# Optimization experiments

Hardware: AMD Instinct MI355X
Metric: run time of the kernel (lower is better)

The kernel has to match this reference:

```python
import jax, jax.numpy as jnp
import numpy as np

B, X, Y, Z = 8, 128, 128, 128


def setup_inputs() -> dict:
    key = jax.random.key(0)
    k1, k2 = jax.random.split(key)
    mu = jax.random.normal(k1, (B, X, Y, Z), dtype=jnp.float32)
    active = jax.random.uniform(k2, (B, X, Y, Z), dtype=jnp.float32)
    dx = jnp.ones((1,), dtype=jnp.float32)
    return {"mu": mu, "active": active, "dx": dx}


def _lap_kernel(mu, active, dx):
    # mu, active: [X, Y, Z] single-sample grids; dx: scalar
    mu_eff = mu * active
    lap = (jnp.roll(mu_eff, 1, 0) + jnp.roll(mu_eff, -1, 0)
           + jnp.roll(mu_eff, 1, 1) + jnp.roll(mu_eff, -1, 1)
           + jnp.roll(mu_eff, 1, 2) + jnp.roll(mu_eff, -1, 2)
           - 6.0 * mu_eff) / dx ** 2
    return lap * active


def reference(mu, active, dx):
    # Faithful to Node.proces_collection: gather fields by pattern, then
    # vmap the runnable with in_axes=(0, 0, None) over the batch axis.
    out = jax.vmap(_lap_kernel, in_axes=(0, 0, None))(mu, active, dx[0])
    return out
```

## Files before the change

kernel.cpp:

```cpp
#include <hip/hip_runtime.h>

#define NB 8
#define NX 128
#define NY 128
#define NZ 128

#define TY 8
#define TX 8
#define XC (NX / TX)
#define YT (NY / TY)
#define PLANE_ROWS (TY + 2)

__global__ __launch_bounds__(256) void lap_lds(
    const float* __restrict__ mu,
    const float* __restrict__ act,
    const float* __restrict__ dxp,
    float* __restrict__ out)
{
    __shared__ float e[3][PLANE_ROWS][NZ];

    const int tid = threadIdx.x;
    const int bid = blockIdx.x;
    const int xc = bid & (XC - 1);
    const int yt = (bid >> 4) & (YT - 1);
    const int b  = bid >> 8;

    const int x0 = xc * TX;
    const int y0 = yt * TY;
    const int planeYZ = NY * NZ;
    const int baseB = b * NX * planeYZ;

    const float dxv = dxp[0];
    const float inv = 1.0f / (dxv * dxv);

    const int r  = tid >> 5;
    const int zq = tid & 31;
    const int z0 = zq * 4;

    float4 A;
    float4 Bt;

    auto load_plane = [&](int gx, int slot, float4* keepA) {
        const int px = baseB + gx * planeYZ;
        {
            const int gIdx = px + (y0 + r) * NZ + z0;
            float4 m = *reinterpret_cast<const float4*>(mu + gIdx);
            float4 a = *reinterpret_cast<const float4*>(act + gIdx);
            *keepA = a;
            float4 ev = make_float4(m.x * a.x, m.y * a.y, m.z * a.z, m.w * a.w);
            *reinterpret_cast<float4*>(&e[slot][r + 1][z0]) = ev;
        }
        if (tid < 64) {
            const int hr = tid >> 5;
            const int hzq = tid & 31;
            const int gy = hr ? ((y0 + TY) & (NY - 1)) : ((y0 - 1) & (NY - 1));
            const int lr = hr ? (TY + 1) : 0;
            const int gIdx = px + gy * NZ + hzq * 4;
            float4 m = *reinterpret_cast<const float4*>(mu + gIdx);
            float4 a = *reinterpret_cast<const float4*>(act + gIdx);
            float4 ev = make_float4(m.x * a.x, m.y * a.y, m.z * a.z, m.w * a.w);
            *reinterpret_cast<float4*>(&e[slot][lr][hzq * 4]) = ev;
        }
    };

    load_plane((x0 - 1) & (NX - 1), 0, &Bt);
    load_plane(x0, 1, &A);

    for (int i = 0; i < TX; ++i) {
        const int sm = i % 3;
        const int sc = (i + 1) % 3;
        const int sp = (i + 2) % 3;

        load_plane((x0 + i + 1) & (NX - 1), sp, &Bt);
        __syncthreads();

        const int gx = x0 + i;
        const int px = baseB + gx * planeYZ;
        {
            float4 ec  = *reinterpret_cast<const float4*>(&e[sc][r + 1][z0]);
            float4 exm = *reinterpret_cast<const float4*>(&e[sm][r + 1][z0]);
            float4 exP = *reinterpret_cast<const float4*>(&e[sp][r + 1][z0]);
            float4 eym = *reinterpret_cast<const float4*>(&e[sc][r][z0]);
            float4 eyp = *reinterpret_cast<const float4*>(&e[sc][r + 2][z0]);
            float ezm = e[sc][r + 1][(z0 - 1) & (NZ - 1)];
            float ezp = e[sc][r + 1][(z0 + 4) & (NZ - 1)];
            float4 o;
            o.x = (exm.x + exP.x + eym.x + eyp.x + ezm + ec.y - 6.0f * ec.x) * inv * A.x;
            o.y = (exm.y + exP.y + eym.y + eyp.y + ec.x + ec.z - 6.0f * ec.y) * inv * A.y;
            o.z = (exm.z + exP.z + eym.z + eyp.z + ec.y + ec.w - 6.0f * ec.z) * inv * A.z;
            o.w = (exm.w + exP.w + eym.w + eyp.w + ec.z + ezp - 6.0f * ec.w) * inv * A.w;
            const int gIdx = px + (y0 + r) * NZ + z0;
            *reinterpret_cast<float4*>(out + gIdx) = o;
        }

        A = Bt;
        __syncthreads();
    }
}

extern "C" void kernel_launch(void* const* d_in, const int* in_sizes, int n_in,
                              void* d_out, int out_size, void* d_ws, size_t ws_size,
                              hipStream_t stream) {
    const float* mu  = (const float*)d_in[0];
    const float* act = (const float*)d_in[1];
    const float* dx  = (const float*)d_in[2];
    float* out = (float*)d_out;

    const int grid = NB * YT * XC;
    lap_lds<<<grid, 256, 0, stream>>>(mu, act, dx, out);
}
```

Before: 40.57 us.

## March x-planes in registers with double-buffered LDS and larger tiles

Each thread now keeps its previous, current and next x-plane values in registers instead of a triple-buffered LDS array. LDS is cut to a double buffer used only for y-neighbours, and z-neighbours come from warp shuffles. Tiles grow to 16x16 with 512 threads, which lowers the relative halo reload overhead. In exchange there is one fewer barrier per plane, more register pressure, fewer blocks in the grid, and the next-plane load is exposed within each iteration.

```diff
diff --git a/kernel.cpp b/kernel.cpp
--- a/kernel.cpp
+++ b/kernel.cpp
@@ -5,25 +5,25 @@
 #define NY 128
 #define NZ 128
 
-#define TY 8
-#define TX 8
+#define TY 16
+#define TX 16
 #define XC (NX / TX)
 #define YT (NY / TY)
-#define PLANE_ROWS (TY + 2)
+#define ROWS (TY + 2)
 
-__global__ __launch_bounds__(256) void lap_lds(
+__global__ __launch_bounds__(512) void lap_march(
     const float* __restrict__ mu,
     const float* __restrict__ act,
     const float* __restrict__ dxp,
     float* __restrict__ out)
 {
-    __shared__ float e[3][PLANE_ROWS][NZ];
+    __shared__ float buf[2][ROWS][NZ];
 
     const int tid = threadIdx.x;
     const int bid = blockIdx.x;
     const int xc = bid & (XC - 1);
-    const int yt = (bid >> 4) & (YT - 1);
-    const int b  = bid >> 8;
+    const int yt = (bid >> 3) & (YT - 1);
+    const int b  = bid >> 6;
 
     const int x0 = xc * TX;
     const int y0 = yt * TY;
@@ -36,64 +36,64 @@
     const int r  = tid >> 5;
     const int zq = tid & 31;
     const int z0 = zq * 4;
+    const int gy = y0 + r;
 
-    float4 A;
-    float4 Bt;
+    float4 eP, eC, eN, aC, aN;
 
-    auto load_plane = [&](int gx, int slot, float4* keepA) {
-        const int px = baseB + gx * planeYZ;
-        {
-            const int gIdx = px + (y0 + r) * NZ + z0;
+    auto ldE = [&](int gx, float4* ev, float4* av) {
+        const int gIdx = baseB + gx * planeYZ + gy * NZ + z0;
+        float4 m = *reinterpret_cast<const float4*>(mu + gIdx);
+        float4 a = *reinterpret_cast<const float4*>(act + gIdx);
+        *av = a;
+        *ev = make_float4(m.x * a.x, m.y * a.y, m.z * a.z, m.w * a.w);
+    };
+
+    auto ldHalo = [&](int gx, int slot) {
+        if (tid < 64) {
+            const int hr = tid >> 5;
+            const int hz = (tid & 31) * 4;
+            const int hy = hr ? ((y0 + TY) & (NY - 1)) : ((y0 - 1) & (NY - 1));
+            const int gIdx = baseB + gx * planeYZ + hy * NZ + hz;
             float4 m = *reinterpret_cast<const float4*>(mu + gIdx);
             float4 a = *reinterpret_cast<const float4*>(act + gIdx);
-            *keepA = a;
-            float4 ev = make_float4(m.x * a.x, m.y * a.y, m.z * a.z, m.w * a.w);
-            *reinterpret_cast<float4*>(&e[slot][r + 1][z0]) = ev;
-        }
-        if (tid < 64) {
-            const int hr = tid >> 5;
-            const int hzq = tid & 31;
-            const int gy = hr ? ((y0 + TY) & (NY - 1)) : ((y0 - 1) & (NY - 1));
-            const int lr = hr ? (TY + 1) : 0;
-            const int gIdx = px + gy * NZ + hzq * 4;
-            float4 m = *reinterpret_cast<const float4*>(mu + gIdx);
-            float4 a = *reinterpret_cast<const float4*>(act + gIdx);
-            float4 ev = make_float4(m.x * a.x, m.y * a.y, m.z * a.z, m.w * a.w);
-            *reinterpret_cast<float4*>(&e[slot][lr][hzq * 4]) = ev;
+            *reinterpret_cast<float4*>(&buf[slot][hr ? TY + 1 : 0][hz]) =
+                make_float4(m.x * a.x, m.y * a.y, m.z * a.z, m.w * a.w);
         }
     };
 
-    load_plane((x0 - 1) & (NX - 1), 0, &Bt);
-    load_plane(x0, 1, &A);
+    {
+        float4 dummy;
+        ldE((x0 - 1) & (NX - 1), &eP, &dummy);
+        ldE(x0, &eC, &aC);
+        *reinterpret_cast<float4*>(&buf[0][r + 1][z0]) = eC;
+        ldHalo(x0, 0);
+    }
+    __syncthreads();
 
     for (int i = 0; i < TX; ++i) {
-        const int sm = i % 3;
-        const int sc = (i + 1) % 3;
-        const int sp = (i + 2) % 3;
-
-        load_plane((x0 + i + 1) & (NX - 1), sp, &Bt);
-        __syncthreads();
-
-        const int gx = x0 + i;
-        const int px = baseB + gx * planeYZ;
-        {
-            float4 ec  = *reinterpret_cast<const float4*>(&e[sc][r + 1][z0]);
-            float4 exm = *reinterpret_cast<const float4*>(&e[sm][r + 1][z0]);
-            float4 exP = *reinterpret_cast<const float4*>(&e[sp][r + 1][z0]);
-            float4 eym = *reinterpret_cast<const float4*>(&e[sc][r][z0]);
-            float4 eyp = *reinterpret_cast<const float4*>(&e[sc][r + 2][z0]);
-            float ezm = e[sc][r + 1][(z0 - 1) & (NZ - 1)];
-            float ezp = e[sc][r + 1][(z0 + 4) & (NZ - 1)];
-            float4 o;
-            o.x = (exm.x + exP.x + eym.x + eyp.x + ezm + ec.y - 6.0f * ec.x) * inv * A.x;
-            o.y = (exm.y + exP.y + eym.y + eyp.y + ec.x + ec.z - 6.0f * ec.y) * inv * A.y;
-            o.z = (exm.z + exP.z + eym.z + eyp.z + ec.y + ec.w - 6.0f * ec.z) * inv * A.z;
-            o.w = (exm.w + exP.w + eym.w + eyp.w + ec.z + ezp - 6.0f * ec.w) * inv * A.w;
-            const int gIdx = px + (y0 + r) * NZ + z0;
-            *reinterpret_cast<float4*>(out + gIdx) = o;
+        const int gxn = (x0 + i + 1) & (NX - 1);
+        ldE(gxn, &eN, &aN);
+        if (i < TX - 1) {
+            *reinterpret_cast<float4*>(&buf[(i + 1) & 1][r + 1][z0]) = eN;
+            ldHalo(gxn, (i + 1) & 1);
         }
 
-        A = Bt;
+        const int s = i & 1;
+        float4 eym = *reinterpret_cast<const float4*>(&buf[s][r][z0]);
+        float4 eyp = *reinterpret_cast<const float4*>(&buf[s][r + 2][z0]);
+        float ezm = __shfl(eC.w, (zq + 31) & 31, 32);
+        float ezp = __shfl(eC.x, (zq + 1) & 31, 32);
+
+        float4 o;
+        o.x = (eP.x + eN.x + eym.x + eyp.x + ezm  + eC.y - 6.0f * eC.x) * inv * aC.x;
+        o.y = (eP.y + eN.y + eym.y + eyp.y + eC.x + eC.z - 6.0f * eC.y) * inv * aC.y;
+        o.z = (eP.z + eN.z + eym.z + eyp.z + eC.y + eC.w - 6.0f * eC.z) * inv * aC.z;
+        o.w = (eP.w + eN.w + eym.w + eyp.w + eC.z + ezp  - 6.0f * eC.w) * inv * aC.w;
+
+        const int gIdx = baseB + (x0 + i) * planeYZ + gy * NZ + z0;
+        *reinterpret_cast<float4*>(out + gIdx) = o;
+
+        eP = eC; eC = eN; aC = aN;
         __syncthreads();
     }
 }
@@ -107,5 +107,5 @@
     float* out = (float*)d_out;
 
     const int grid = NB * YT * XC;
-    lap_lds<<<grid, 256, 0, stream>>>(mu, act, dx, out);
+    lap_march<<<grid, 512, 0, stream>>>(mu, act, dx, out);
 }
```

Result: faster. 36.10 us (-11.0%).
